# Optimization experiments

Measured on AMD Instinct MI355X. Metric: run time of the kernel, lower is better.

## Reference

```python
import jax, jax.numpy as jnp
import numpy as np

NIN = 512
HID = 512
T = 512
B = 64
INITRANGE = 0.1


def setup_inputs() -> dict:
    key = jax.random.key(0)
    ks = jax.random.split(key, 6)
    x = jax.random.normal(ks[0], (T, B, NIN), dtype=jnp.float32)
    mask = jnp.ones((T, B), dtype=jnp.float32)
    # torch Linear(nin+hidden, hidden): weight [HID, NIN+HID], uniform(-0.1, 0.1), bias zeros
    def lin(k):
        return jax.random.uniform(k, (HID, NIN + HID), dtype=jnp.float32,
                                  minval=-INITRANGE, maxval=INITRANGE)
    return {
        "x": x, "mask": mask,
        "Wf": lin(ks[1]), "bf": jnp.zeros((HID,), jnp.float32),
        "Wi": lin(ks[2]), "bi": jnp.zeros((HID,), jnp.float32),
        "Wc": lin(ks[3]), "bc": jnp.zeros((HID,), jnp.float32),
        "Wo": lin(ks[4]), "bo": jnp.zeros((HID,), jnp.float32),
    }


def reference(x, mask, Wf, bf, Wi, bi, Wc, bc, Wo, bo):
    # Fuse the 4 gate linears into one GEMM per step (same math).
    # Gate order: f, i, o, ctilde
    W = jnp.concatenate([Wf, Wi, Wo, Wc], axis=0)        # [4H, NIN+H]
    b = jnp.concatenate([bf, bi, bo, bc], axis=0)        # [4H]
    H = Wf.shape[0]
    Bsz = x.shape[1]
    h0 = jnp.zeros((Bsz, H), x.dtype)
    c0 = jnp.zeros((Bsz, H), x.dtype)

    def step(carry, inp):
        h, c = carry
        xt, mt = inp                                    # [B, NIN], [B]
        comb = jnp.concatenate([h, xt], axis=1)         # hidden first, as in torch code
        z = comb @ W.T + b                              # [B, 4H]
        f = jax.nn.sigmoid(z[:, 0 * H:1 * H])
        i = jax.nn.sigmoid(z[:, 1 * H:2 * H])
        o = jax.nn.sigmoid(z[:, 2 * H:3 * H])
        c_tilde = jnp.tanh(z[:, 3 * H:4 * H])
        m = mt[:, None]
        c_new = f * c + i * c_tilde
        c_new = m * c_new + (1.0 - m) * c
        h_new = o * jnp.tanh(c_new)
        h_new = m * h_new + (1.0 - m) * h
        return (h_new, c_new), (h_new, i)

    (_, _), (h_hist, i_hist) = jax.lax.scan(step, (h0, c0), (x, mask))
    return h_hist, i_hist  # each [T, B, H]
```

## Files before the change

kernel.cpp:

```cpp
#include <hip/hip_runtime.h>
#include <math.h>

#define T_STEPS 512
#define BATCH   64
#define HID     512
#define NROW    2048
#define HHIST   16777216ULL

__device__ __forceinline__ float sigf(float z) {
  z = fminf(fmaxf(z, -30.f), 30.f);
  return 1.f / (1.f + __expf(-z));
}
__device__ __forceinline__ float tanhf_(float v) {
  v = fminf(fmaxf(v, -15.f), 15.f);
  const float e = __expf(2.f * v);
  return (e - 1.f) / (e + 1.f);
}

__global__ __launch_bounds__(256) void xgemm_kernel(
    const float* __restrict__ x,
    const float* __restrict__ Wf, const float* __restrict__ Wi,
    const float* __restrict__ Wo, const float* __restrict__ Wc,
    const float* __restrict__ bf, const float* __restrict__ bi,
    const float* __restrict__ bo, const float* __restrict__ bc,
    float* __restrict__ Zx)
{
  const int rtile = blockIdx.x;
  const int t     = blockIdx.y;
  const int g  = rtile >> 2;
  const int n0 = (rtile & 3) * 128;
  const float* Wg = (g == 0) ? Wf : (g == 1) ? Wi : (g == 2) ? Wo : Wc;
  const float* bg = (g == 0) ? bf : (g == 1) ? bi : (g == 2) ? bo : bc;

  __shared__ float Wt[32][132];
  __shared__ float Xt[32][68];

  const int tid = threadIdx.x;
  const int tr  = tid & 31;
  const int tb  = tid >> 5;

  float acc[4][8];
#pragma unroll
  for (int i = 0; i < 4; ++i)
#pragma unroll
    for (int j = 0; j < 8; ++j) acc[i][j] = 0.f;

  float biasv[4];
#pragma unroll
  for (int i = 0; i < 4; ++i) biasv[i] = bg[n0 + tr * 4 + i];

  const float* xt = x + (size_t)t * (BATCH * 512);

  for (int kc = 0; kc < 512; kc += 32) {
#pragma unroll
    for (int p = 0; p < 4; ++p) {
      const int r  = p * 32 + (tid >> 3);
      const int kk = (tid & 7) * 4;
      float4 v = *(const float4*)&Wg[(size_t)(n0 + r) * 1024 + 512 + kc + kk];
      Wt[kk + 0][r] = v.x; Wt[kk + 1][r] = v.y;
      Wt[kk + 2][r] = v.z; Wt[kk + 3][r] = v.w;
    }
    {
      const int b  = tid >> 2;
      const int kk = (tid & 3) * 8;
      float4 v0 = *(const float4*)&xt[b * 512 + kc + kk];
      float4 v1 = *(const float4*)&xt[b * 512 + kc + kk + 4];
      Xt[kk + 0][b] = v0.x; Xt[kk + 1][b] = v0.y;
      Xt[kk + 2][b] = v0.z; Xt[kk + 3][b] = v0.w;
      Xt[kk + 4][b] = v1.x; Xt[kk + 5][b] = v1.y;
      Xt[kk + 6][b] = v1.z; Xt[kk + 7][b] = v1.w;
    }
    __syncthreads();
#pragma unroll
    for (int kk = 0; kk < 32; ++kk) {
      float4 wv = *(const float4*)&Wt[kk][tr * 4];
      float4 x0 = *(const float4*)&Xt[kk][tb * 8];
      float4 x1 = *(const float4*)&Xt[kk][tb * 8 + 4];
      const float wa[4] = {wv.x, wv.y, wv.z, wv.w};
      const float xa[8] = {x0.x, x0.y, x0.z, x0.w, x1.x, x1.y, x1.z, x1.w};
#pragma unroll
      for (int i = 0; i < 4; ++i)
#pragma unroll
        for (int j = 0; j < 8; ++j)
          acc[i][j] = fmaf(wa[i], xa[j], acc[i][j]);
    }
    __syncthreads();
  }

  const int rg = g * 512 + n0 + tr * 4;
#pragma unroll
  for (int ir = 0; ir < 4; ++ir) {
    const float bv = biasv[ir];
    float4 o0 = make_float4(acc[ir][0] + bv, acc[ir][1] + bv,
                            acc[ir][2] + bv, acc[ir][3] + bv);
    float4 o1 = make_float4(acc[ir][4] + bv, acc[ir][5] + bv,
                            acc[ir][6] + bv, acc[ir][7] + bv);
    float* dst = Zx + (((size_t)t * 8 + tb) * NROW + rg + ir) * 8;
    *(float4*)dst       = o0;
    *(float4*)(dst + 4) = o1;
  }
}

__global__ __launch_bounds__(512, 2) void lstm_rec_fast(
    const float* __restrict__ mask,
    const float* __restrict__ Wf, const float* __restrict__ Wi,
    const float* __restrict__ Wo, const float* __restrict__ Wc,
    const float* __restrict__ Zx,
    unsigned long long* __restrict__ hP,
    float* __restrict__ out)
{
  __shared__ float hlds[4096];

  const int tid  = threadIdx.x;
  const int w    = blockIdx.x;
  const int g    = w & 7;
  const int ib   = w >> 3;
  const int wv   = tid >> 6;
  const int lane = tid & 63;

  const int unit0 = ib * 16 + wv * 2;
  const int g4l = lane >> 4;
  const int u2l = (lane >> 3) & 1;
  const int bl  = lane & 7;

  float Wreg[8][8];
  {
    const float* Wm[4] = {Wf, Wi, Wo, Wc};
#pragma unroll
    for (int g4 = 0; g4 < 4; ++g4)
#pragma unroll
      for (int u2 = 0; u2 < 2; ++u2) {
        const float* row = Wm[g4] + (size_t)(unit0 + u2) * 1024 + lane * 8;
        float4 a = *(const float4*)row;
        float4 b = *(const float4*)(row + 4);
        float* Wr = Wreg[g4 * 2 + u2];
        Wr[0] = a.x; Wr[1] = a.y; Wr[2] = a.z; Wr[3] = a.w;
        Wr[4] = b.x; Wr[5] = b.y; Wr[6] = b.z; Wr[7] = b.w;
      }
  }

  float c_r = 0.f, h_r = 0.f;
  const int base16 = lane << 4;

  for (int t = 0; t < T_STEPS; ++t) {
    const float zpre = Zx[(((size_t)t * 8 + g) * NROW +
                           g4l * 512 + unit0 + u2l) * 8 + bl];
    const float mval = mask[t * 64 + g * 8 + bl];

    __syncthreads();

    {
      unsigned long long* hq =
          hP + ((size_t)((t & 1) * 8 + g) * 512 + tid) * 8;
      unsigned long long q[8];
      while (true) {
#pragma unroll
        for (int j = 0; j < 8; ++j)
          q[j] = __hip_atomic_load(hq + j, __ATOMIC_RELAXED,
                                   __HIP_MEMORY_SCOPE_AGENT);
        bool ok = true;
#pragma unroll
        for (int j = 0; j < 8; ++j)
          ok &= ((unsigned)(q[j] >> 32) == (unsigned)t);
        if (ok) break;
        __builtin_amdgcn_s_sleep(1);
      }
      float4 lo = make_float4(__uint_as_float((unsigned)q[0]),
                              __uint_as_float((unsigned)q[1]),
                              __uint_as_float((unsigned)q[2]),
                              __uint_as_float((unsigned)q[3]));
      float4 hi = make_float4(__uint_as_float((unsigned)q[4]),
                              __uint_as_float((unsigned)q[5]),
                              __uint_as_float((unsigned)q[6]),
                              __uint_as_float((unsigned)q[7]));
      const int s0 = tid * 2, s1 = s0 + 1;
      const int p0 = (s0 & ~7) | ((s0 + (s0 >> 4)) & 7);
      const int p1 = (s1 & ~7) | ((s1 + (s1 >> 4)) & 7);
      *(float4*)&hlds[p0 * 4] = lo;
      *(float4*)&hlds[p1 * 4] = hi;
    }
    __syncthreads();

    float v[64];
    {
      const int s0 = base16, s1 = s0 + 1;
      const int p0 = (s0 & ~7) | ((s0 + lane) & 7);
      const int p1 = (s1 & ~7) | ((s1 + lane) & 7);
      const float4 h0 = *(const float4*)&hlds[p0 * 4];
      const float4 h1 = *(const float4*)&hlds[p1 * 4];
#pragma unroll
      for (int r = 0; r < 8; ++r) {
        const float wr = Wreg[r][0];
        v[r * 8 + 0] = wr * h0.x;  v[r * 8 + 1] = wr * h0.y;
        v[r * 8 + 2] = wr * h0.z;  v[r * 8 + 3] = wr * h0.w;
        v[r * 8 + 4] = wr * h1.x;  v[r * 8 + 5] = wr * h1.y;
        v[r * 8 + 6] = wr * h1.z;  v[r * 8 + 7] = wr * h1.w;
      }
    }
#pragma unroll
    for (int j = 1; j < 8; ++j) {
      const int s0 = base16 + 2 * j, s1 = s0 + 1;
      const int p0 = (s0 & ~7) | ((s0 + lane) & 7);
      const int p1 = (s1 & ~7) | ((s1 + lane) & 7);
      const float4 h0 = *(const float4*)&hlds[p0 * 4];
      const float4 h1 = *(const float4*)&hlds[p1 * 4];
#pragma unroll
      for (int r = 0; r < 8; ++r) {
        const float wr = Wreg[r][j];
        v[r * 8 + 0] = fmaf(wr, h0.x, v[r * 8 + 0]);
        v[r * 8 + 1] = fmaf(wr, h0.y, v[r * 8 + 1]);
        v[r * 8 + 2] = fmaf(wr, h0.z, v[r * 8 + 2]);
        v[r * 8 + 3] = fmaf(wr, h0.w, v[r * 8 + 3]);
        v[r * 8 + 4] = fmaf(wr, h1.x, v[r * 8 + 4]);
        v[r * 8 + 5] = fmaf(wr, h1.y, v[r * 8 + 5]);
        v[r * 8 + 6] = fmaf(wr, h1.z, v[r * 8 + 6]);
        v[r * 8 + 7] = fmaf(wr, h1.w, v[r * 8 + 7]);
      }
    }

#pragma unroll
    for (int m = 0; m < 6; ++m) {
      const int lb = (lane >> m) & 1;
#pragma unroll
      for (int p = 0; p < (32 >> m); ++p) {
        const float keep = lb ? v[2 * p + 1] : v[2 * p];
        const float send = lb ? v[2 * p]     : v[2 * p + 1];
        v[p] = keep + __shfl_xor(send, 1 << m, 64);
      }
    }
    const float z = v[0] + zpre;

    const float zi_ = __shfl(z, lane + 16, 64);
    const float zo_ = __shfl(z, lane + 32, 64);
    const float zc_ = __shfl(z, lane + 48, 64);

    const float f  = sigf(z);
    const float ig = sigf(zi_);
    const float o  = sigf(zo_);
    const float ct = tanhf_(zc_);
    float cn = f * c_r + ig * ct;
    cn = mval * cn + (1.f - mval) * c_r;
    float hn = o * tanhf_(cn);
    hn = mval * hn + (1.f - mval) * h_r;

    if (lane < 16) {
      c_r = cn; h_r = hn;
      const int n = unit0 + u2l;
      const size_t hidx = ((size_t)(((t + 1) & 1) * 8 + g) * 512 + n) * 8 + bl;
      const unsigned long long pk =
          ((unsigned long long)(unsigned)(t + 1) << 32) |
          (unsigned long long)__float_as_uint(hn);
      __hip_atomic_store(hP + hidx, pk, __ATOMIC_RELAXED,
                         __HIP_MEMORY_SCOPE_AGENT);
      const size_t ob = ((size_t)t * 64 + g * 8 + bl) * 512 + n;
      __builtin_nontemporal_store(hn, &out[ob]);
      __builtin_nontemporal_store(ig, &out[HHIST + ob]);
    }
  }
}

__device__ __forceinline__ void grid_barrier(unsigned* cnt, int w, int tid, int round) {
  __syncthreads();
  if (tid == 0) {
    __builtin_amdgcn_fence(__ATOMIC_RELEASE, "agent");
    unsigned* gc = cnt + 16 + ((w >> 4) << 5);
    unsigned prev = __hip_atomic_fetch_add(gc, 1u, __ATOMIC_RELAXED,
                                           __HIP_MEMORY_SCOPE_AGENT);
    if ((prev & 15u) == 15u)
      __hip_atomic_fetch_add(cnt, 1u, __ATOMIC_RELAXED,
                             __HIP_MEMORY_SCOPE_AGENT);
    const unsigned target = (unsigned)(round + 1) * 16u;
    while (__hip_atomic_load(cnt, __ATOMIC_RELAXED,
                             __HIP_MEMORY_SCOPE_AGENT) < target)
      __builtin_amdgcn_s_sleep(2);
    __builtin_amdgcn_fence(__ATOMIC_ACQUIRE, "agent");
  }
  __syncthreads();
}

__global__ __launch_bounds__(512) void lstm_rec_inline(
    const float* __restrict__ x,  const float* __restrict__ mask,
    const float* __restrict__ Wf, const float* __restrict__ Wi,
    const float* __restrict__ Wo, const float* __restrict__ Wc,
    const float* __restrict__ bf, const float* __restrict__ bi,
    const float* __restrict__ bo, const float* __restrict__ bc,
    float* __restrict__ hT, unsigned* __restrict__ cnt,
    float* __restrict__ out)
{
  constexpr int WC = 1024;
  __shared__ float Wlds[8 * WC];
  __shared__ float zpart[8 * 8 * 64];

  const int tid = threadIdx.x;
  const int w   = blockIdx.x;
  const int kq  = tid >> 6;
  const int b   = tid & 63;
  const int n0  = ((w & 7) << 6) + ((w >> 3) << 1);

#pragma unroll
  for (int i = 0; i < WC / 256; ++i) {
    const int idx4 = tid + (i << 9);
    const int rr   = idx4 / (WC / 4);
    const int col  = (idx4 % (WC / 4)) * 4;
    const int g = rr >> 1, u = rr & 1;
    const float* Wrow =
        ((g == 0) ? Wf : (g == 1) ? Wi : (g == 2) ? Wo : Wc) +
        (size_t)(n0 + u) * 1024;
    *(float4*)&Wlds[rr * WC + col] = *(const float4*)&Wrow[col];
  }

  float biasv[4] = {0.f, 0.f, 0.f, 0.f};
  float c_r = 0.f, h_r = 0.f;
  if (tid < 128) {
    const int u = tid >> 6;
    biasv[0] = bf[n0 + u]; biasv[1] = bi[n0 + u];
    biasv[2] = bo[n0 + u]; biasv[3] = bc[n0 + u];
  }
  __syncthreads();

  for (int t = 0; t < T_STEPS; ++t) {
    float zpre[4] = {0.f, 0.f, 0.f, 0.f};
    float mval = 0.f;
    if (tid < 128) {
      const int bb = tid & 63;
      mval = mask[t * 64 + bb];
#pragma unroll
      for (int g = 0; g < 4; ++g) zpre[g] = biasv[g];
    }

    float acc[8];
#pragma unroll
    for (int rr = 0; rr < 8; ++rr) acc[rr] = 0.f;

    {
      const float* hcur = hT + ((t & 1) << 15);
      const int k0 = kq << 6;
#pragma unroll
      for (int k4 = 0; k4 < 16; ++k4) {
        const int k = k0 + (k4 << 2);
        const float h0 = hcur[(k + 0) * 64 + b];
        const float h1 = hcur[(k + 1) * 64 + b];
        const float h2 = hcur[(k + 2) * 64 + b];
        const float h3 = hcur[(k + 3) * 64 + b];
#pragma unroll
        for (int rr = 0; rr < 8; ++rr) {
          float4 wv = *(const float4*)&Wlds[rr * WC + k];
          acc[rr] = fmaf(h0, wv.x, acc[rr]);
          acc[rr] = fmaf(h1, wv.y, acc[rr]);
          acc[rr] = fmaf(h2, wv.z, acc[rr]);
          acc[rr] = fmaf(h3, wv.w, acc[rr]);
        }
      }
    }
    {
      const float* xt = x + (size_t)t * (64 * 512) + b * 512;
      const int k0 = kq << 6;
#pragma unroll
      for (int k4 = 0; k4 < 16; ++k4) {
        const int k = k0 + (k4 << 2);
        float4 xv = *(const float4*)&xt[k];
#pragma unroll
        for (int rr = 0; rr < 8; ++rr) {
          float4 wv = *(const float4*)&Wlds[rr * WC + 512 + k];
          acc[rr] = fmaf(xv.x, wv.x, acc[rr]);
          acc[rr] = fmaf(xv.y, wv.y, acc[rr]);
          acc[rr] = fmaf(xv.z, wv.z, acc[rr]);
          acc[rr] = fmaf(xv.w, wv.w, acc[rr]);
        }
      }
    }

#pragma unroll
    for (int rr = 0; rr < 8; ++rr)
      zpart[((kq << 3) + rr) * 64 + b] = acc[rr];
    __syncthreads();

    if (tid < 128) {
      const int u = tid >> 6, bb = tid & 63;
      float z[4];
#pragma unroll
      for (int g = 0; g < 4; ++g) {
        const int rr = g * 2 + u;
        float s = zpre[g];
#pragma unroll
        for (int q = 0; q < 8; ++q) s += zpart[((q << 3) + rr) * 64 + bb];
        z[g] = s;
      }
      const float f  = sigf(z[0]);
      const float ig = sigf(z[1]);
      const float o  = sigf(z[2]);
      const float ct = tanhf_(z[3]);
      float cn = f * c_r + ig * ct;
      cn = mval * cn + (1.f - mval) * c_r;
      c_r = cn;
      float hn = o * tanhf_(cn);
      hn = mval * hn + (1.f - mval) * h_r;
      h_r = hn;
      const int n = n0 + u;
      hT[(((t + 1) & 1) << 15) + n * 64 + bb] = hn;
      out[((size_t)t * 64 + bb) * 512 + n]         = hn;
      out[HHIST + ((size_t)t * 64 + bb) * 512 + n] = ig;
    }

    if (t != T_STEPS - 1) grid_barrier(cnt, w, tid, t);
  }
}

extern "C" void kernel_launch(void* const* d_in, const int* in_sizes, int n_in,
                              void* d_out, int out_size, void* d_ws, size_t ws_size,
                              hipStream_t stream) {
  (void)in_sizes; (void)n_in; (void)out_size;
  const float* x    = (const float*)d_in[0];
  const float* mask = (const float*)d_in[1];
  const float* Wf   = (const float*)d_in[2];
  const float* bf   = (const float*)d_in[3];
  const float* Wi   = (const float*)d_in[4];
  const float* bi   = (const float*)d_in[5];
  const float* Wc   = (const float*)d_in[6];
  const float* bc   = (const float*)d_in[7];
  const float* Wo   = (const float*)d_in[8];
  const float* bo   = (const float*)d_in[9];
  float* out = (float*)d_out;

  const size_t zx_bytes = (size_t)T_STEPS * NROW * 64 * 4;
  const size_t hp_bytes = (size_t)2 * 8 * 512 * 8 * 8;
  const bool fast = ws_size >= zx_bytes + hp_bytes;

  if (fast) {
    float* Zx = (float*)d_ws;
    unsigned long long* hP = (unsigned long long*)((char*)d_ws + zx_bytes);
    hipMemsetAsync(hP, 0, hp_bytes, stream);
    hipLaunchKernelGGL(xgemm_kernel, dim3(16, 512), dim3(256), 0, stream,
                       x, Wf, Wi, Wo, Wc, bf, bi, bo, bc, Zx);
    void* kargs[] = { (void*)&mask, (void*)&Wf, (void*)&Wi, (void*)&Wo,
                      (void*)&Wc, (void*)&Zx, (void*)&hP, (void*)&out };
    hipLaunchCooperativeKernel(reinterpret_cast<void*>(&lstm_rec_fast),
                               dim3(256), dim3(512), kargs, 0, stream);
  } else {
    float* hT = (float*)d_ws;
    const size_t h_bytes = 2 * 64 * 512 * 4;
    unsigned* cnt = (unsigned*)((char*)hT + h_bytes);
    hipMemsetAsync(hT, 0, h_bytes + 4096, stream);
    void* kargs[] = { (void*)&x, (void*)&mask, (void*)&Wf, (void*)&Wi,
                      (void*)&Wo, (void*)&Wc, (void*)&bf, (void*)&bi,
                      (void*)&bo, (void*)&bc, (void*)&hT, (void*)&cnt,
                      (void*)&out };
    hipLaunchCooperativeKernel(reinterpret_cast<void*>(&lstm_rec_inline),
                               dim3(256), dim3(512), kargs, 0, stream);
  }
}
```

Measured before the change: 3.782 ms.

## Move recurrent matvec onto bf16 MFMA with split hi/lo precision

Replaces the per-lane FP32 FMA matvec and shuffle reduction in the recurrent kernel with bf16 MFMA 16x16x32 instructions. Weights and hidden state are split into bf16 hi and lo parts (three MFMAs per tile) to keep close to FP32 accuracy. The batch is regrouped into 4 groups of 16 across 128 blocks, and the Zx and hP layouts change to match. This is meant to cut per-step compute and the reduction latency, at the cost of extra LDS traffic, a packing step, and some precision loss from the split-bf16 emulation.

```diff
diff --git a/kernel.cpp b/kernel.cpp
--- a/kernel.cpp
+++ b/kernel.cpp
@@ -7,6 +7,14 @@
 #define NROW    2048
 #define HHIST   16777216ULL
 
+#define GROUPS  4
+#define GB      16
+#define UW      16
+#define WPG     32
+
+typedef __attribute__((ext_vector_type(8))) short short8_t;
+typedef __attribute__((ext_vector_type(4))) float float4_t;
+
 __device__ __forceinline__ float sigf(float z) {
   z = fminf(fmaxf(z, -30.f), 30.f);
   return 1.f / (1.f + __expf(-z));
@@ -15,6 +23,18 @@
   v = fminf(fmaxf(v, -15.f), 15.f);
   const float e = __expf(2.f * v);
   return (e - 1.f) / (e + 1.f);
+}
+__device__ __forceinline__ unsigned short bf16hi(float f) {
+  unsigned u = __float_as_uint(f);
+  return (unsigned short)((u + 0x7fffu + ((u >> 16) & 1u)) >> 16);
+}
+__device__ __forceinline__ float bf16f(unsigned short h) {
+  return __uint_as_float(((unsigned)h) << 16);
+}
+__device__ __forceinline__ unsigned packh(float f) {
+  unsigned short h = bf16hi(f);
+  unsigned short l = bf16hi(f - bf16f(h));
+  return (((unsigned)h) << 16) | (unsigned)l;
 }
 
 __global__ __launch_bounds__(256) void xgemm_kernel(
@@ -95,7 +115,8 @@
                             acc[ir][2] + bv, acc[ir][3] + bv);
     float4 o1 = make_float4(acc[ir][4] + bv, acc[ir][5] + bv,
                             acc[ir][6] + bv, acc[ir][7] + bv);
-    float* dst = Zx + (((size_t)t * 8 + tb) * NROW + rg + ir) * 8;
+    float* dst = Zx + ((((size_t)t * 4 + (tb >> 1)) * NROW + rg + ir) * 16 +
+                       (tb & 1) * 8);
     *(float4*)dst       = o0;
     *(float4*)(dst + 4) = o1;
   }
@@ -109,150 +130,142 @@
     unsigned long long* __restrict__ hP,
     float* __restrict__ out)
 {
-  __shared__ float hlds[4096];
+  __shared__ __align__(16) short hip_[16 * 512];
+  __shared__ __align__(16) short lop_[16 * 512];
+  __shared__ float zp[4][2][16][17];
 
   const int tid  = threadIdx.x;
   const int w    = blockIdx.x;
-  const int g    = w & 7;
-  const int ib   = w >> 3;
+  const int g    = w & 3;
+  const int iw   = w >> 2;
+  const int n0   = iw * UW;
+
   const int wv   = tid >> 6;
   const int lane = tid & 63;
-
-  const int unit0 = ib * 16 + wv * 2;
-  const int g4l = lane >> 4;
-  const int u2l = (lane >> 3) & 1;
-  const int bl  = lane & 7;
-
-  float Wreg[8][8];
-  {
-    const float* Wm[4] = {Wf, Wi, Wo, Wc};
-#pragma unroll
-    for (int g4 = 0; g4 < 4; ++g4)
-#pragma unroll
-      for (int u2 = 0; u2 < 2; ++u2) {
-        const float* row = Wm[g4] + (size_t)(unit0 + u2) * 1024 + lane * 8;
-        float4 a = *(const float4*)row;
-        float4 b = *(const float4*)(row + 4);
-        float* Wr = Wreg[g4 * 2 + u2];
-        Wr[0] = a.x; Wr[1] = a.y; Wr[2] = a.z; Wr[3] = a.w;
-        Wr[4] = b.x; Wr[5] = b.y; Wr[6] = b.z; Wr[7] = b.w;
-      }
-  }
-
+  const int gmt  = wv >> 1;
+  const int kh   = wv & 1;
+  const int kb   = lane >> 4;
+  const int l15  = lane & 15;
+
+  const float* Wm4 = (gmt == 0) ? Wf : (gmt == 1) ? Wi : (gmt == 2) ? Wo : Wc;
+  const float* Wrow = Wm4 + (size_t)(n0 + l15) * 1024;
+  short8_t Ahi[8], Alo[8];
+#pragma unroll
+  for (int w8 = 0; w8 < 8; ++w8) {
+    const int base = kh * 256 + w8 * 32 + kb * 8;
+#pragma unroll
+    for (int j = 0; j < 8; ++j) {
+      const float f = Wrow[base + j];
+      const unsigned short h = bf16hi(f);
+      Ahi[w8][j] = (short)h;
+      Alo[w8][j] = (short)bf16hi(f - bf16f(h));
+    }
+  }
+
+  const int b_e = tid >> 4, u_e = tid & 15;
   float c_r = 0.f, h_r = 0.f;
-  const int base16 = lane << 4;
+
+  const int b_s = tid >> 5;
+  const int kr  = (tid & 31) * 16;
+  char* hib = (char*)hip_;
+  char* lob = (char*)lop_;
+  const int rowS = b_s * 1024;
+  const int xrS  = (b_s & 7) << 4;
+  const int oS   = kr * 2;
+
+  const int rowB = l15 * 1024;
+  const int xrB  = (l15 & 7) << 4;
 
   for (int t = 0; t < T_STEPS; ++t) {
-    const float zpre = Zx[(((size_t)t * 8 + g) * NROW +
-                           g4l * 512 + unit0 + u2l) * 8 + bl];
-    const float mval = mask[t * 64 + g * 8 + bl];
-
-    __syncthreads();
+    float zxv[4]; float mval = 0.f;
+    if (tid < 256) {
+      mval = mask[t * 64 + g * GB + b_e];
+#pragma unroll
+      for (int g4 = 0; g4 < 4; ++g4)
+        zxv[g4] = Zx[(((size_t)t * 4 + g) * NROW + g4 * 512 + n0 + u_e) * 16 + b_e];
+    }
 
     {
       unsigned long long* hq =
-          hP + ((size_t)((t & 1) * 8 + g) * 512 + tid) * 8;
-      unsigned long long q[8];
+          hP + ((((size_t)(t & 1) * 4 + g) * 16 + b_s) * 512 + kr);
+      unsigned p[16];
       while (true) {
-#pragma unroll
-        for (int j = 0; j < 8; ++j)
+        unsigned long long q[16];
+#pragma unroll
+        for (int j = 0; j < 16; ++j)
           q[j] = __hip_atomic_load(hq + j, __ATOMIC_RELAXED,
                                    __HIP_MEMORY_SCOPE_AGENT);
         bool ok = true;
 #pragma unroll
-        for (int j = 0; j < 8; ++j)
+        for (int j = 0; j < 16; ++j)
           ok &= ((unsigned)(q[j] >> 32) == (unsigned)t);
-        if (ok) break;
+        if (ok) {
+#pragma unroll
+          for (int j = 0; j < 16; ++j) p[j] = (unsigned)q[j];
+          break;
+        }
         __builtin_amdgcn_s_sleep(1);
       }
-      float4 lo = make_float4(__uint_as_float((unsigned)q[0]),
-                              __uint_as_float((unsigned)q[1]),
-                              __uint_as_float((unsigned)q[2]),
-                              __uint_as_float((unsigned)q[3]));
-      float4 hi = make_float4(__uint_as_float((unsigned)q[4]),
-                              __uint_as_float((unsigned)q[5]),
-                              __uint_as_float((unsigned)q[6]),
-                              __uint_as_float((unsigned)q[7]));
-      const int s0 = tid * 2, s1 = s0 + 1;
-      const int p0 = (s0 & ~7) | ((s0 + (s0 >> 4)) & 7);
-      const int p1 = (s1 & ~7) | ((s1 + (s1 >> 4)) & 7);
-      *(float4*)&hlds[p0 * 4] = lo;
-      *(float4*)&hlds[p1 * 4] = hi;
+      short8_t H0, H1, L0, L1;
+#pragma unroll
+      for (int j = 0; j < 8; ++j) {
+        H0[j] = (short)(p[j] >> 16);     L0[j] = (short)(p[j] & 0xffffu);
+        H1[j] = (short)(p[j + 8] >> 16); L1[j] = (short)(p[j + 8] & 0xffffu);
+      }
+      const int pa = (lane & 1) << 4;
+      *(short8_t*)(hib + rowS + ((oS + pa) ^ xrS))        = (lane & 1) ? H1 : H0;
+      *(short8_t*)(hib + rowS + ((oS + (pa ^ 16)) ^ xrS)) = (lane & 1) ? H0 : H1;
+      *(short8_t*)(lob + rowS + ((oS + pa) ^ xrS))        = (lane & 1) ? L1 : L0;
+      *(short8_t*)(lob + rowS + ((oS + (pa ^ 16)) ^ xrS)) = (lane & 1) ? L0 : L1;
     }
     __syncthreads();
 
-    float v[64];
     {
-      const int s0 = base16, s1 = s0 + 1;
-      const int p0 = (s0 & ~7) | ((s0 + lane) & 7);
-      const int p1 = (s1 & ~7) | ((s1 + lane) & 7);
-      const float4 h0 = *(const float4*)&hlds[p0 * 4];
-      const float4 h1 = *(const float4*)&hlds[p1 * 4];
-#pragma unroll
-      for (int r = 0; r < 8; ++r) {
-        const float wr = Wreg[r][0];
-        v[r * 8 + 0] = wr * h0.x;  v[r * 8 + 1] = wr * h0.y;
-        v[r * 8 + 2] = wr * h0.z;  v[r * 8 + 3] = wr * h0.w;
-        v[r * 8 + 4] = wr * h1.x;  v[r * 8 + 5] = wr * h1.y;
-        v[r * 8 + 6] = wr * h1.z;  v[r * 8 + 7] = wr * h1.w;
-      }
-    }
-#pragma unroll
-    for (int j = 1; j < 8; ++j) {
-      const int s0 = base16 + 2 * j, s1 = s0 + 1;
-      const int p0 = (s0 & ~7) | ((s0 + lane) & 7);
-      const int p1 = (s1 & ~7) | ((s1 + lane) & 7);
-      const float4 h0 = *(const float4*)&hlds[p0 * 4];
-      const float4 h1 = *(const float4*)&hlds[p1 * 4];
-#pragma unroll
-      for (int r = 0; r < 8; ++r) {
-        const float wr = Wreg[r][j];
-        v[r * 8 + 0] = fmaf(wr, h0.x, v[r * 8 + 0]);
-        v[r * 8 + 1] = fmaf(wr, h0.y, v[r * 8 + 1]);
-        v[r * 8 + 2] = fmaf(wr, h0.z, v[r * 8 + 2]);
-        v[r * 8 + 3] = fmaf(wr, h0.w, v[r * 8 + 3]);
-        v[r * 8 + 4] = fmaf(wr, h1.x, v[r * 8 + 4]);
-        v[r * 8 + 5] = fmaf(wr, h1.y, v[r * 8 + 5]);
-        v[r * 8 + 6] = fmaf(wr, h1.z, v[r * 8 + 6]);
-        v[r * 8 + 7] = fmaf(wr, h1.w, v[r * 8 + 7]);
-      }
-    }
-
-#pragma unroll
-    for (int m = 0; m < 6; ++m) {
-      const int lb = (lane >> m) & 1;
-#pragma unroll
-      for (int p = 0; p < (32 >> m); ++p) {
-        const float keep = lb ? v[2 * p + 1] : v[2 * p];
-        const float send = lb ? v[2 * p]     : v[2 * p + 1];
-        v[p] = keep + __shfl_xor(send, 1 << m, 64);
-      }
-    }
-    const float z = v[0] + zpre;
-
-    const float zi_ = __shfl(z, lane + 16, 64);
-    const float zo_ = __shfl(z, lane + 32, 64);
-    const float zc_ = __shfl(z, lane + 48, 64);
-
-    const float f  = sigf(z);
-    const float ig = sigf(zi_);
-    const float o  = sigf(zo_);
-    const float ct = tanhf_(zc_);
-    float cn = f * c_r + ig * ct;
-    cn = mval * cn + (1.f - mval) * c_r;
-    float hn = o * tanhf_(cn);
-    hn = mval * hn + (1.f - mval) * h_r;
-
-    if (lane < 16) {
-      c_r = cn; h_r = hn;
-      const int n = unit0 + u2l;
-      const size_t hidx = ((size_t)(((t + 1) & 1) * 8 + g) * 512 + n) * 8 + bl;
+      float4_t c0 = {0.f, 0.f, 0.f, 0.f}, c1 = {0.f, 0.f, 0.f, 0.f};
+#pragma unroll
+      for (int w8 = 0; w8 < 8; ++w8) {
+        const int o = kh * 512 + w8 * 64 + kb * 16;
+        const short8_t bh = *(const short8_t*)(hib + rowB + (o ^ xrB));
+        const short8_t bl = *(const short8_t*)(lob + rowB + (o ^ xrB));
+        if (w8 & 1) {
+          c1 = __builtin_amdgcn_mfma_f32_16x16x32_bf16(Ahi[w8], bh, c1, 0, 0, 0);
+          c1 = __builtin_amdgcn_mfma_f32_16x16x32_bf16(Ahi[w8], bl, c1, 0, 0, 0);
+          c1 = __builtin_amdgcn_mfma_f32_16x16x32_bf16(Alo[w8], bh, c1, 0, 0, 0);
+        } else {
+          c0 = __builtin_amdgcn_mfma_f32_16x16x32_bf16(Ahi[w8], bh, c0, 0, 0, 0);
+          c0 = __builtin_amdgcn_mfma_f32_16x16x32_bf16(Ahi[w8], bl, c0, 0, 0, 0);
+          c0 = __builtin_amdgcn_mfma_f32_16x16x32_bf16(Alo[w8], bh, c0, 0, 0, 0);
+        }
+      }
+#pragma unroll
+      for (int r = 0; r < 4; ++r)
+        zp[gmt][kh][kb * 4 + r][l15] = c0[r] + c1[r];
+    }
+    __syncthreads();
+
+    if (tid < 256) {
+      float z[4];
+#pragma unroll
+      for (int g4 = 0; g4 < 4; ++g4)
+        z[g4] = zxv[g4] + zp[g4][0][u_e][b_e] + zp[g4][1][u_e][b_e];
+      const float f  = sigf(z[0]);
+      const float ig = sigf(z[1]);
+      const float o  = sigf(z[2]);
+      const float ct = tanhf_(z[3]);
+      float cn = f * c_r + ig * ct;
+      cn = mval * cn + (1.f - mval) * c_r;
+      c_r = cn;
+      float hn = o * tanhf_(cn);
+      hn = mval * hn + (1.f - mval) * h_r;
+      h_r = hn;
+      const size_t hidx =
+          (((size_t)((t + 1) & 1) * 4 + g) * 16 + b_e) * 512 + (n0 + u_e);
       const unsigned long long pk =
-          ((unsigned long long)(unsigned)(t + 1) << 32) |
-          (unsigned long long)__float_as_uint(hn);
+          (((unsigned long long)(unsigned)(t + 1)) << 32) |
+          (unsigned long long)packh(hn);
       __hip_atomic_store(hP + hidx, pk, __ATOMIC_RELAXED,
                          __HIP_MEMORY_SCOPE_AGENT);
-      const size_t ob = ((size_t)t * 64 + g * 8 + bl) * 512 + n;
+      const size_t ob = ((size_t)t * 64 + g * GB + b_e) * 512 + (n0 + u_e);
       __builtin_nontemporal_store(hn, &out[ob]);
       __builtin_nontemporal_store(ig, &out[HHIST + ob]);
     }
@@ -423,7 +436,7 @@
   float* out = (float*)d_out;
 
   const size_t zx_bytes = (size_t)T_STEPS * NROW * 64 * 4;
-  const size_t hp_bytes = (size_t)2 * 8 * 512 * 8 * 8;
+  const size_t hp_bytes = (size_t)2 * GROUPS * GB * 512 * 8;
   const bool fast = ws_size >= zx_bytes + hp_bytes;
 
   if (fast) {
@@ -435,7 +448,7 @@
     void* kargs[] = { (void*)&mask, (void*)&Wf, (void*)&Wi, (void*)&Wo,
                       (void*)&Wc, (void*)&Zx, (void*)&hP, (void*)&out };
     hipLaunchCooperativeKernel(reinterpret_cast<void*>(&lstm_rec_fast),
-                               dim3(256), dim3(512), kargs, 0, stream);
+                               dim3(128), dim3(512), kargs, 0, stream);
   } else {
     float* hT = (float*)d_ws;
     const size_t h_bytes = 2 * 64 * 512 * 4;
```

Result: slower. 5.943 ms (+57.1%).
